# Performance work log

Hardware: AMD Instinct MI355X
Metric: run time of the kernel (lower is better)

The kernel has to match this reference:

```python
import jax, jax.numpy as jnp
import numpy as np

D = 8       # q_dim / embed dim
NF = 8      # num_feats
OUT = 8     # out_dim


def _get_emb(sin_inp):
    # interleaved sin/cos, matching positional_encodings.get_emb
    return jnp.stack([jnp.sin(sin_inp), jnp.cos(sin_inp)], axis=-1).reshape(sin_inp.shape[0], -1)


def pos_encoding_2d(X, Y, ch, dtype=jnp.float32):
    # PositionalEncoding2D over dims (X=window, Y=num_feats), channels=ch
    c = int(np.ceil(ch / 4) * 2)
    inv_freq = jnp.asarray((1.0 / (10000.0 ** (np.arange(0, c, 2) / np.float32(c)))).astype(np.float32))
    emb_x = _get_emb(jnp.arange(X, dtype=dtype)[:, None] * inv_freq[None, :])  # (X, c)
    emb_y = _get_emb(jnp.arange(Y, dtype=dtype)[:, None] * inv_freq[None, :])  # (Y, c)
    emb = jnp.zeros((X, Y, 2 * c), dtype)
    emb = emb.at[:, :, :c].set(emb_x[:, None, :])
    emb = emb.at[:, :, c:2 * c].set(emb_y[None, :, :])
    return emb[:, :, :ch]


def layer_norm(x, g, b, eps=1e-5):
    mu = jnp.mean(x, axis=-1, keepdims=True)
    var = jnp.mean((x - mu) ** 2, axis=-1, keepdims=True)
    return (x - mu) * jax.lax.rsqrt(var + eps) * g + b


def setup_inputs() -> dict:
    key = jax.random.key(0)
    ks = jax.random.split(key, 12)
    B, W = 128, 2048
    x = jax.random.normal(ks[0], (B, W, NF), dtype=jnp.float32)
    m = jax.random.randint(ks[1], (B, W, NF), 0, 2, dtype=jnp.int32)
    m = m.at[:, :, 0].set(0)  # guarantee at least one unmasked key per row
    s = 0.1
    return {
        "x": x,
        "m": m,
        "emb_w": jax.random.normal(ks[2], (D, 1), jnp.float32) * s,
        "emb_b": jax.random.normal(ks[3], (D,), jnp.float32) * s,
        "emb_ln_g": jnp.ones((D,), jnp.float32),
        "emb_ln_b": jnp.zeros((D,), jnp.float32),
        "ln_g": jnp.ones((D,), jnp.float32),
        "ln_b": jnp.zeros((D,), jnp.float32),
        "var_query": jax.random.normal(ks[4], (1, 1, D), jnp.float32) * s,
        "in_proj_w": jax.random.normal(ks[5], (3 * D, D), jnp.float32) * s,
        "in_proj_b": jax.random.normal(ks[6], (3 * D,), jnp.float32) * s,
        "out_proj_w": jax.random.normal(ks[7], (D, D), jnp.float32) * s,
        "out_proj_b": jax.random.normal(ks[8], (D,), jnp.float32) * s,
        "proj_w": jax.random.normal(ks[9], (OUT, D), jnp.float32) * s,
        "proj_b": jax.random.normal(ks[10], (OUT,), jnp.float32) * s,
    }


def reference(x, m, emb_w, emb_b, emb_ln_g, emb_ln_b, ln_g, ln_b, var_query,
              in_proj_w, in_proj_b, out_proj_w, out_proj_b, proj_w, proj_b):
    B, W, F = x.shape
    d = emb_w.shape[0]
    # LinearEmbed: Linear(1, d) on each scalar, then LayerNorm(d)
    h = x[..., None] * emb_w[:, 0] + emb_b              # (B, W, F, d)
    h = layer_norm(h, emb_ln_g, emb_ln_b)
    # 2D positional encoding over (window, feature) dims
    h = h + pos_encoding_2d(W, F, d)[None]
    # pre-attention LayerNorm
    h = layer_norm(h, ln_g, ln_b)
    # single-query multihead (1 head) cross attention, key_padding_mask = m
    Wq, Wk, Wv = in_proj_w[:d], in_proj_w[d:2 * d], in_proj_w[2 * d:]
    bq, bk, bv = in_proj_b[:d], in_proj_b[d:2 * d], in_proj_b[2 * d:]
    qv = Wq @ var_query.reshape(d) + bq                 # (d,) shared query
    k = jnp.einsum('bwfd,ed->bwfe', h, Wk) + bk         # (B, W, F, d)
    v = jnp.einsum('bwfd,ed->bwfe', h, Wv) + bv         # (B, W, F, d)
    logits = jnp.einsum('bwfe,e->bwf', k, qv) / jnp.sqrt(jnp.float32(d))
    logits = jnp.where(m.astype(bool), -jnp.inf, logits)
    attn_w = jax.nn.softmax(logits, axis=-1)            # (B, W, F)
    attn = jnp.einsum('bwf,bwfe->bwe', attn_w, v)       # (B, W, d)
    attn = attn @ out_proj_w.T + out_proj_b
    # final projection
    out = attn @ proj_w.T + proj_b                      # (B, W, OUT)
    return out
```

## Files before the change

kernel.cpp:

```cpp
#include <hip/hip_runtime.h>
#include <math.h>

#define THREADS 256
#define W_DIM 2048
#define INV_SQRT8 0.35355339059327373f

__global__ __launch_bounds__(THREADS) void misstsm_fused(
    const float* __restrict__ x, const int* __restrict__ m,
    const float* __restrict__ emb_w, const float* __restrict__ emb_b,
    const float* __restrict__ emb_ln_g, const float* __restrict__ emb_ln_b,
    const float* __restrict__ ln_g, const float* __restrict__ ln_b,
    const float* __restrict__ var_query,
    const float* __restrict__ in_proj_w, const float* __restrict__ in_proj_b,
    const float* __restrict__ out_proj_w, const float* __restrict__ out_proj_b,
    const float* __restrict__ proj_w, const float* __restrict__ proj_b,
    float* __restrict__ out, int npos)
{
    __shared__ float s_M[64];
    __shared__ float s_c2[8];
    __shared__ float s_a[8], s_bb[8], s_wlg[8], s_lg[8];
    __shared__ float s_Bf[32];
    __shared__ float s_sc[5];

    const int t = threadIdx.x;

    if (t < 64) {
        const int p = t >> 3, d = t & 7;
        float acc = 0.0f;
        #pragma unroll
        for (int e = 0; e < 8; ++e) {
            float po = 0.0f;
            #pragma unroll
            for (int o = 0; o < 8; ++o) po = fmaf(proj_w[p*8+o], out_proj_w[o*8+e], po);
            acc = fmaf(po, in_proj_w[(16+e)*8 + d], acc);
        }
        s_M[t] = acc;
    } else if (t < 72) {
        const int d = t - 64;
        float wk = 0.0f;
        #pragma unroll
        for (int e = 0; e < 8; ++e) {
            float qe = in_proj_b[e];
            #pragma unroll
            for (int dd = 0; dd < 8; ++dd) qe = fmaf(in_proj_w[e*8+dd], var_query[dd], qe);
            wk = fmaf(in_proj_w[(8+e)*8 + d], qe, wk);
        }
        s_wlg[d] = ln_g[d] * wk * INV_SQRT8;
        s_lg[d]  = ln_g[d];
    } else if (t < 80) {
        const int d = t - 72;
        float ewm = 0.0f, ebm = 0.0f;
        #pragma unroll
        for (int dd = 0; dd < 8; ++dd) { ewm += emb_w[dd]; ebm += emb_b[dd]; }
        ewm *= 0.125f; ebm *= 0.125f;
        s_a[d]  = (emb_w[d] - ewm) * emb_ln_g[d];
        s_bb[d] = (emb_b[d] - ebm) * emb_ln_g[d];
    } else if (t < 88) {
        const int p = t - 80;
        float c = proj_b[p];
        #pragma unroll
        for (int o = 0; o < 8; ++o) {
            float ob2 = out_proj_b[o];
            #pragma unroll
            for (int e = 0; e < 8; ++e) ob2 = fmaf(out_proj_w[o*8+e], in_proj_b[16+e], ob2);
            c = fmaf(proj_w[p*8+o], ob2, c);
        }
        #pragma unroll
        for (int e = 0; e < 8; ++e) {
            float po = 0.0f;
            #pragma unroll
            for (int o = 0; o < 8; ++o) po = fmaf(proj_w[p*8+o], out_proj_w[o*8+e], po);
            #pragma unroll
            for (int d = 0; d < 8; ++d)
                c = fmaf(po * in_proj_w[(16+e)*8 + d], ln_b[d], c);
        }
        s_c2[p] = c;
    } else if (t < 120) {
        const int k = t - 88, f = k >> 2, j = k & 3;
        const float ff = (float)f;
        float tr;
        if      (j == 0) tr = sinf(ff);
        else if (j == 1) tr = cosf(ff);
        else if (j == 2) tr = sinf(0.01f * ff);
        else             tr = cosf(0.01f * ff);
        s_Bf[k] = emb_ln_b[4 + j] + tr;
    } else if (t == 120) {
        float ewm = 0.0f, ebm = 0.0f;
        #pragma unroll
        for (int d = 0; d < 8; ++d) { ewm += emb_w[d]; ebm += emb_b[d]; }
        ewm *= 0.125f; ebm *= 0.125f;
        float A = 0.0f, Bc = 0.0f, Cc = 0.0f;
        #pragma unroll
        for (int d = 0; d < 8; ++d) {
            const float dw = emb_w[d] - ewm, db = emb_b[d] - ebm;
            A = fmaf(dw, dw, A); Bc = fmaf(dw, db, Bc); Cc = fmaf(db, db, Cc);
        }
        s_sc[0] = A * 0.125f;
        s_sc[1] = 2.0f * Bc * 0.125f;
        s_sc[2] = Cc * 0.125f + 1e-5f;
    } else if (t == 121) {
        float qv[8];
        float bkq = 0.0f;
        #pragma unroll
        for (int e = 0; e < 8; ++e) {
            float qe = in_proj_b[e];
            #pragma unroll
            for (int dd = 0; dd < 8; ++dd) qe = fmaf(in_proj_w[e*8+dd], var_query[dd], qe);
            qv[e] = qe;
            bkq = fmaf(in_proj_b[8+e], qe, bkq);
        }
        float swlg = 0.0f, ckd = 0.0f;
        #pragma unroll
        for (int d = 0; d < 8; ++d) {
            float wk = 0.0f;
            #pragma unroll
            for (int e = 0; e < 8; ++e) wk = fmaf(in_proj_w[(8+e)*8 + d], qv[e], wk);
            swlg = fmaf(ln_g[d], wk, swlg);
            ckd  = fmaf(ln_b[d], wk, ckd);
        }
        s_sc[3] = swlg * INV_SQRT8;
        s_sc[4] = (ckd + bkq) * INV_SQRT8;
    }
    __syncthreads();

    const int pos = blockIdx.x * THREADS + t;
    if (pos >= npos) return;
    const int w = pos & (W_DIM - 1);

    const float4* xv4 = reinterpret_cast<const float4*>(x);
    const int4*   mv4 = reinterpret_cast<const int4*>(m);
    const float4 xa = xv4[pos*2+0];
    const float4 xb = xv4[pos*2+1];
    const int4   ma = mv4[pos*2+0];
    const int4   mb = mv4[pos*2+1];

    const float xf[8] = {xa.x, xa.y, xa.z, xa.w, xb.x, xb.y, xb.z, xb.w};
    const int mk = (ma.x!=0?1:0) | (ma.y!=0?2:0) | (ma.z!=0?4:0) | (ma.w!=0?8:0)
                 | (mb.x!=0?16:0) | (mb.y!=0?32:0) | (mb.z!=0?64:0) | (mb.w!=0?128:0);

    const float fw = (float)w;
    float pB[4];
    pB[0] = emb_ln_b[0] + sinf(fw);
    pB[1] = emb_ln_b[1] + cosf(fw);
    pB[2] = emb_ln_b[2] + sinf(0.01f * fw);
    pB[3] = emb_ln_b[3] + cosf(0.01f * fw);

    const float A    = s_sc[0];
    const float twoB = s_sc[1];
    const float Cc   = s_sc[2];
    const float swlg = s_sc[3];
    const float cK   = s_sc[4];

    float av[8];
    #pragma unroll
    for (int d = 0; d < 8; ++d) av[d] = 0.0f;
    float S = 0.0f, smu = 0.0f;

    #pragma unroll
    for (int f = 0; f < 8; ++f) {
        const float xs = xf[f];
        const float r  = rsqrtf(fmaf(xs, fmaf(xs, A, twoB), Cc));
        const float tt = xs * r;
        float v[8];
        #pragma unroll
        for (int j = 0; j < 4; ++j)
            v[j] = fmaf(tt, s_a[j], fmaf(r, s_bb[j], pB[j]));
        #pragma unroll
        for (int j = 0; j < 4; ++j)
            v[4+j] = fmaf(tt, s_a[4+j], fmaf(r, s_bb[4+j], s_Bf[f*4 + j]));
        float sv = 0.0f, s2 = 0.0f, dt = 0.0f;
        #pragma unroll
        for (int d = 0; d < 8; ++d) {
            sv += v[d];
            s2  = fmaf(v[d], v[d], s2);
            dt  = fmaf(v[d], s_wlg[d], dt);
        }
        const float mu  = sv * 0.125f;
        const float var = fmaf(-mu, mu, fmaf(s2, 0.125f, 1e-5f));
        const float r2  = rsqrtf(var);
        const float l   = fmaf(r2, fmaf(-mu, swlg, dt), cK);
        const float e   = __expf(l);
        const float pp  = ((mk >> f) & 1) ? 0.0f : e;
        S += pp;
        const float cf = pp * r2;
        #pragma unroll
        for (int d = 0; d < 8; ++d) av[d] = fmaf(cf, v[d], av[d]);
        smu = fmaf(cf, mu, smu);
    }

    const float invS = 1.0f / S;
    float q[8];
    #pragma unroll
    for (int d = 0; d < 8; ++d) q[d] = s_lg[d] * invS * (av[d] - smu);

    float o[8];
    #pragma unroll
    for (int p = 0; p < 8; ++p) {
        float dp = s_c2[p];
        #pragma unroll
        for (int d = 0; d < 8; ++d) dp = fmaf(s_M[p*8+d], q[d], dp);
        o[p] = dp;
    }
    float4* ov4 = reinterpret_cast<float4*>(out);
    ov4[pos*2+0] = make_float4(o[0], o[1], o[2], o[3]);
    ov4[pos*2+1] = make_float4(o[4], o[5], o[6], o[7]);
}

extern "C" void kernel_launch(void* const* d_in, const int* in_sizes, int n_in,
                              void* d_out, int out_size, void* d_ws, size_t ws_size,
                              hipStream_t stream) {
    const float* x          = (const float*)d_in[0];
    const int*   m          = (const int*)d_in[1];
    const float* emb_w      = (const float*)d_in[2];
    const float* emb_b      = (const float*)d_in[3];
    const float* emb_ln_g   = (const float*)d_in[4];
    const float* emb_ln_b   = (const float*)d_in[5];
    const float* ln_g       = (const float*)d_in[6];
    const float* ln_b       = (const float*)d_in[7];
    const float* var_query  = (const float*)d_in[8];
    const float* in_proj_w  = (const float*)d_in[9];
    const float* in_proj_b  = (const float*)d_in[10];
    const float* out_proj_w = (const float*)d_in[11];
    const float* out_proj_b = (const float*)d_in[12];
    const float* proj_w     = (const float*)d_in[13];
    const float* proj_b     = (const float*)d_in[14];
    float* out = (float*)d_out;

    const int npos = in_sizes[0] / 8;
    const int grid = (npos + THREADS - 1) / THREADS;
    misstsm_fused<<<grid, THREADS, 0, stream>>>(
        x, m, emb_w, emb_b, emb_ln_g, emb_ln_b, ln_g, ln_b, var_query,
        in_proj_w, in_proj_b, out_proj_w, out_proj_b, proj_w, proj_b,
        out, npos);
}
```

Baseline: 16.00 us.

## Algebraically precompute LN statistics per feature and hoist global loads before setup

The per-feature second LayerNorm mean, variance and logit dot product are rewritten as closed-form polynomials in (tt, r), using per-block precomputed coefficients and per-feature tables in shared memory. This removes the 8-wide v vector and its reductions from the inner loop. The attention accumulator is kept as a few scalar sums and reassembled after the loop. The x/m global loads are also issued before the setup phase so they overlap with it, and sin/cos are merged into sincosf. The cost is more setup work per block, possible out-of-bounds loads for tail threads since the bounds check now comes after the loads, and variance computed by expansion, which risks cancellation.

```diff
diff --git a/kernel.cpp b/kernel.cpp
--- a/kernel.cpp
+++ b/kernel.cpp
@@ -19,113 +19,11 @@
     __shared__ float s_M[64];
     __shared__ float s_c2[8];
     __shared__ float s_a[8], s_bb[8], s_wlg[8], s_lg[8];
-    __shared__ float s_Bf[32];
-    __shared__ float s_sc[5];
+    __shared__ float s_F[8][12];
+    __shared__ float s_sc[12];
 
     const int t = threadIdx.x;
-
-    if (t < 64) {
-        const int p = t >> 3, d = t & 7;
-        float acc = 0.0f;
-        #pragma unroll
-        for (int e = 0; e < 8; ++e) {
-            float po = 0.0f;
-            #pragma unroll
-            for (int o = 0; o < 8; ++o) po = fmaf(proj_w[p*8+o], out_proj_w[o*8+e], po);
-            acc = fmaf(po, in_proj_w[(16+e)*8 + d], acc);
-        }
-        s_M[t] = acc;
-    } else if (t < 72) {
-        const int d = t - 64;
-        float wk = 0.0f;
-        #pragma unroll
-        for (int e = 0; e < 8; ++e) {
-            float qe = in_proj_b[e];
-            #pragma unroll
-            for (int dd = 0; dd < 8; ++dd) qe = fmaf(in_proj_w[e*8+dd], var_query[dd], qe);
-            wk = fmaf(in_proj_w[(8+e)*8 + d], qe, wk);
-        }
-        s_wlg[d] = ln_g[d] * wk * INV_SQRT8;
-        s_lg[d]  = ln_g[d];
-    } else if (t < 80) {
-        const int d = t - 72;
-        float ewm = 0.0f, ebm = 0.0f;
-        #pragma unroll
-        for (int dd = 0; dd < 8; ++dd) { ewm += emb_w[dd]; ebm += emb_b[dd]; }
-        ewm *= 0.125f; ebm *= 0.125f;
-        s_a[d]  = (emb_w[d] - ewm) * emb_ln_g[d];
-        s_bb[d] = (emb_b[d] - ebm) * emb_ln_g[d];
-    } else if (t < 88) {
-        const int p = t - 80;
-        float c = proj_b[p];
-        #pragma unroll
-        for (int o = 0; o < 8; ++o) {
-            float ob2 = out_proj_b[o];
-            #pragma unroll
-            for (int e = 0; e < 8; ++e) ob2 = fmaf(out_proj_w[o*8+e], in_proj_b[16+e], ob2);
-            c = fmaf(proj_w[p*8+o], ob2, c);
-        }
-        #pragma unroll
-        for (int e = 0; e < 8; ++e) {
-            float po = 0.0f;
-            #pragma unroll
-            for (int o = 0; o < 8; ++o) po = fmaf(proj_w[p*8+o], out_proj_w[o*8+e], po);
-            #pragma unroll
-            for (int d = 0; d < 8; ++d)
-                c = fmaf(po * in_proj_w[(16+e)*8 + d], ln_b[d], c);
-        }
-        s_c2[p] = c;
-    } else if (t < 120) {
-        const int k = t - 88, f = k >> 2, j = k & 3;
-        const float ff = (float)f;
-        float tr;
-        if      (j == 0) tr = sinf(ff);
-        else if (j == 1) tr = cosf(ff);
-        else if (j == 2) tr = sinf(0.01f * ff);
-        else             tr = cosf(0.01f * ff);
-        s_Bf[k] = emb_ln_b[4 + j] + tr;
-    } else if (t == 120) {
-        float ewm = 0.0f, ebm = 0.0f;
-        #pragma unroll
-        for (int d = 0; d < 8; ++d) { ewm += emb_w[d]; ebm += emb_b[d]; }
-        ewm *= 0.125f; ebm *= 0.125f;
-        float A = 0.0f, Bc = 0.0f, Cc = 0.0f;
-        #pragma unroll
-        for (int d = 0; d < 8; ++d) {
-            const float dw = emb_w[d] - ewm, db = emb_b[d] - ebm;
-            A = fmaf(dw, dw, A); Bc = fmaf(dw, db, Bc); Cc = fmaf(db, db, Cc);
-        }
-        s_sc[0] = A * 0.125f;
-        s_sc[1] = 2.0f * Bc * 0.125f;
-        s_sc[2] = Cc * 0.125f + 1e-5f;
-    } else if (t == 121) {
-        float qv[8];
-        float bkq = 0.0f;
-        #pragma unroll
-        for (int e = 0; e < 8; ++e) {
-            float qe = in_proj_b[e];
-            #pragma unroll
-            for (int dd = 0; dd < 8; ++dd) qe = fmaf(in_proj_w[e*8+dd], var_query[dd], qe);
-            qv[e] = qe;
-            bkq = fmaf(in_proj_b[8+e], qe, bkq);
-        }
-        float swlg = 0.0f, ckd = 0.0f;
-        #pragma unroll
-        for (int d = 0; d < 8; ++d) {
-            float wk = 0.0f;
-            #pragma unroll
-            for (int e = 0; e < 8; ++e) wk = fmaf(in_proj_w[(8+e)*8 + d], qv[e], wk);
-            swlg = fmaf(ln_g[d], wk, swlg);
-            ckd  = fmaf(ln_b[d], wk, ckd);
-        }
-        s_sc[3] = swlg * INV_SQRT8;
-        s_sc[4] = (ckd + bkq) * INV_SQRT8;
-    }
-    __syncthreads();
-
     const int pos = blockIdx.x * THREADS + t;
-    if (pos >= npos) return;
-    const int w = pos & (W_DIM - 1);
 
     const float4* xv4 = reinterpret_cast<const float4*>(x);
     const int4*   mv4 = reinterpret_cast<const int4*>(m);
@@ -134,64 +32,236 @@
     const int4   ma = mv4[pos*2+0];
     const int4   mb = mv4[pos*2+1];
 
+    if (t < 64) {
+        const int p = t >> 3, d = t & 7;
+        float acc = 0.0f;
+        #pragma unroll
+        for (int e = 0; e < 8; ++e) {
+            float po = 0.0f;
+            #pragma unroll
+            for (int o = 0; o < 8; ++o) po = fmaf(proj_w[p*8+o], out_proj_w[o*8+e], po);
+            acc = fmaf(po, in_proj_w[(16+e)*8 + d], acc);
+        }
+        s_M[t] = acc;
+    } else if (t < 72) {
+        const int d = t - 64;
+        float wk = 0.0f;
+        #pragma unroll
+        for (int e = 0; e < 8; ++e) {
+            float qe = in_proj_b[e];
+            #pragma unroll
+            for (int dd = 0; dd < 8; ++dd) qe = fmaf(in_proj_w[e*8+dd], var_query[dd], qe);
+            wk = fmaf(in_proj_w[(8+e)*8 + d], qe, wk);
+        }
+        s_wlg[d] = ln_g[d] * wk * INV_SQRT8;
+        s_lg[d]  = ln_g[d];
+    } else if (t < 80) {
+        const int d = t - 72;
+        float ewm = 0.0f, ebm = 0.0f;
+        #pragma unroll
+        for (int dd = 0; dd < 8; ++dd) { ewm += emb_w[dd]; ebm += emb_b[dd]; }
+        ewm *= 0.125f; ebm *= 0.125f;
+        s_a[d]  = (emb_w[d] - ewm) * emb_ln_g[d];
+        s_bb[d] = (emb_b[d] - ebm) * emb_ln_g[d];
+    } else if (t == 80) {
+        float ewm = 0.0f, ebm = 0.0f;
+        #pragma unroll
+        for (int d = 0; d < 8; ++d) { ewm += emb_w[d]; ebm += emb_b[d]; }
+        ewm *= 0.125f; ebm *= 0.125f;
+        float A = 0.0f, Bc = 0.0f, Cc = 0.0f;
+        #pragma unroll
+        for (int d = 0; d < 8; ++d) {
+            const float dw = emb_w[d] - ewm, db = emb_b[d] - ebm;
+            A = fmaf(dw, dw, A); Bc = fmaf(dw, db, Bc); Cc = fmaf(db, db, Cc);
+        }
+        s_sc[0] = A * 0.125f;
+        s_sc[1] = 2.0f * Bc * 0.125f;
+        s_sc[2] = Cc * 0.125f + 1e-5f;
+    } else if (t >= 128 && t < 136) {
+        const int p = t - 128;
+        float c = proj_b[p];
+        #pragma unroll
+        for (int o = 0; o < 8; ++o) {
+            float ob2 = out_proj_b[o];
+            #pragma unroll
+            for (int e = 0; e < 8; ++e) ob2 = fmaf(out_proj_w[o*8+e], in_proj_b[16+e], ob2);
+            c = fmaf(proj_w[p*8+o], ob2, c);
+        }
+        #pragma unroll
+        for (int e = 0; e < 8; ++e) {
+            float po = 0.0f;
+            #pragma unroll
+            for (int o = 0; o < 8; ++o) po = fmaf(proj_w[p*8+o], out_proj_w[o*8+e], po);
+            #pragma unroll
+            for (int d = 0; d < 8; ++d)
+                c = fmaf(po * in_proj_w[(16+e)*8 + d], ln_b[d], c);
+        }
+        s_c2[p] = c;
+    } else if (t == 136) {
+        float qv[8]; float bkq = 0.0f;
+        #pragma unroll
+        for (int e = 0; e < 8; ++e) {
+            float qe = in_proj_b[e];
+            #pragma unroll
+            for (int dd = 0; dd < 8; ++dd) qe = fmaf(in_proj_w[e*8+dd], var_query[dd], qe);
+            qv[e] = qe;
+            bkq = fmaf(in_proj_b[8+e], qe, bkq);
+        }
+        float ewm = 0.0f, ebm = 0.0f;
+        #pragma unroll
+        for (int d = 0; d < 8; ++d) { ewm += emb_w[d]; ebm += emb_b[d]; }
+        ewm *= 0.125f; ebm *= 0.125f;
+        float sa = 0, sb = 0, caa = 0, cbb = 0, cab = 0, ca = 0, cb = 0, sw = 0, ck = 0;
+        #pragma unroll
+        for (int d = 0; d < 8; ++d) {
+            const float ad = (emb_w[d] - ewm) * emb_ln_g[d];
+            const float bd = (emb_b[d] - ebm) * emb_ln_g[d];
+            float wk = 0.0f;
+            #pragma unroll
+            for (int e = 0; e < 8; ++e) wk = fmaf(in_proj_w[(8+e)*8 + d], qv[e], wk);
+            const float wl = ln_g[d] * wk * INV_SQRT8;
+            sa += ad; sb += bd;
+            caa = fmaf(ad, ad, caa); cbb = fmaf(bd, bd, cbb); cab = fmaf(ad, bd, cab);
+            ca  = fmaf(ad, wl, ca);  cb  = fmaf(bd, wl, cb);
+            sw += wl;
+            ck  = fmaf(ln_b[d], wk, ck);
+        }
+        s_sc[3]  = sw;
+        s_sc[4]  = (ck + bkq) * INV_SQRT8;
+        s_sc[5]  = sa * 0.125f;
+        s_sc[6]  = sb * 0.125f;
+        s_sc[7]  = caa * 0.125f;
+        s_sc[8]  = cbb * 0.125f;
+        s_sc[9]  = cab * 0.25f;
+        s_sc[10] = ca;
+        s_sc[11] = cb;
+    } else if (t >= 192 && t < 200) {
+        const int f = t - 192;
+        const float ff = (float)f;
+        float sy0, cy0, sy1, cy1;
+        sincosf(ff, &sy0, &cy0);
+        sincosf(0.01f * ff, &sy1, &cy1);
+        float Bf[4];
+        Bf[0] = emb_ln_b[4] + sy0; Bf[1] = emb_ln_b[5] + cy0;
+        Bf[2] = emb_ln_b[6] + sy1; Bf[3] = emb_ln_b[7] + cy1;
+        float ewm = 0.0f, ebm = 0.0f;
+        #pragma unroll
+        for (int d = 0; d < 8; ++d) { ewm += emb_w[d]; ebm += emb_b[d]; }
+        ewm *= 0.125f; ebm *= 0.125f;
+        float qv[8];
+        #pragma unroll
+        for (int e = 0; e < 8; ++e) {
+            float qe = in_proj_b[e];
+            #pragma unroll
+            for (int dd = 0; dd < 8; ++dd) qe = fmaf(in_proj_w[e*8+dd], var_query[dd], qe);
+            qv[e] = qe;
+        }
+        float bsum = 0, aB = 0, bB = 0, b2 = 0, bdot = 0;
+        #pragma unroll
+        for (int j = 0; j < 4; ++j) {
+            const int d = 4 + j;
+            const float ad = (emb_w[d] - ewm) * emb_ln_g[d];
+            const float bd = (emb_b[d] - ebm) * emb_ln_g[d];
+            float wk = 0.0f;
+            #pragma unroll
+            for (int e = 0; e < 8; ++e) wk = fmaf(in_proj_w[(8+e)*8 + d], qv[e], wk);
+            const float wl = ln_g[d] * wk * INV_SQRT8;
+            bsum += Bf[j];
+            aB  = fmaf(ad, Bf[j], aB);
+            bB  = fmaf(bd, Bf[j], bB);
+            b2  = fmaf(Bf[j], Bf[j], b2);
+            bdot = fmaf(wl, Bf[j], bdot);
+            s_F[f][j] = Bf[j];
+        }
+        s_F[f][4] = bsum * 0.125f;
+        s_F[f][5] = aB * 0.25f;
+        s_F[f][6] = bB * 0.25f;
+        s_F[f][7] = b2 * 0.125f;
+        s_F[f][8] = bdot;
+    }
+    __syncthreads();
+
+    if (pos >= npos) return;
+    const int w = pos & (W_DIM - 1);
+
     const float xf[8] = {xa.x, xa.y, xa.z, xa.w, xb.x, xb.y, xb.z, xb.w};
     const int mk = (ma.x!=0?1:0) | (ma.y!=0?2:0) | (ma.z!=0?4:0) | (ma.w!=0?8:0)
                  | (mb.x!=0?16:0) | (mb.y!=0?32:0) | (mb.z!=0?64:0) | (mb.w!=0?128:0);
 
+    const float A    = s_sc[0], twoB = s_sc[1], Cc  = s_sc[2];
+    const float swlg = s_sc[3], cK   = s_sc[4];
+    const float sa8  = s_sc[5], sb8  = s_sc[6];
+    const float caa8 = s_sc[7], cbb8 = s_sc[8], cab8 = s_sc[9];
+    const float ca   = s_sc[10], cb  = s_sc[11];
+
     const float fw = (float)w;
+    float s1, c1, sl, clo;
+    sincosf(fw, &s1, &c1);
+    sincosf(0.01f * fw, &sl, &clo);
     float pB[4];
-    pB[0] = emb_ln_b[0] + sinf(fw);
-    pB[1] = emb_ln_b[1] + cosf(fw);
-    pB[2] = emb_ln_b[2] + sinf(0.01f * fw);
-    pB[3] = emb_ln_b[3] + cosf(0.01f * fw);
-
-    const float A    = s_sc[0];
-    const float twoB = s_sc[1];
-    const float Cc   = s_sc[2];
-    const float swlg = s_sc[3];
-    const float cK   = s_sc[4];
-
-    float av[8];
-    #pragma unroll
-    for (int d = 0; d < 8; ++d) av[d] = 0.0f;
-    float S = 0.0f, smu = 0.0f;
+    pB[0] = emb_ln_b[0] + s1;  pB[1] = emb_ln_b[1] + c1;
+    pB[2] = emb_ln_b[2] + sl;  pB[3] = emb_ln_b[3] + clo;
+
+    float pBsum = 0, apB = 0, bpB = 0, pB2 = 0, pBdot = 0;
+    #pragma unroll
+    for (int j = 0; j < 4; ++j) {
+        pBsum += pB[j];
+        apB  = fmaf(s_a[j],  pB[j], apB);
+        bpB  = fmaf(s_bb[j], pB[j], bpB);
+        pB2  = fmaf(pB[j],  pB[j], pB2);
+        pBdot = fmaf(s_wlg[j], pB[j], pBdot);
+    }
+    const float pBsum8  = pBsum * 0.125f;
+    const float twoapB8 = apB * 0.25f;
+    const float twobpB8 = bpB * 0.25f;
+    const float pB28eps = fmaf(pB2, 0.125f, 1e-5f);
+
+    float S = 0, SC = 0, ctt = 0, crr = 0, smu = 0;
+    float avB[4] = {0, 0, 0, 0};
 
     #pragma unroll
     for (int f = 0; f < 8; ++f) {
+        const float F0 = s_F[f][0], F1 = s_F[f][1], F2 = s_F[f][2], F3 = s_F[f][3];
+        const float F4 = s_F[f][4], F5 = s_F[f][5], F6 = s_F[f][6], F7 = s_F[f][7];
+        const float F8 = s_F[f][8];
         const float xs = xf[f];
         const float r  = rsqrtf(fmaf(xs, fmaf(xs, A, twoB), Cc));
         const float tt = xs * r;
-        float v[8];
-        #pragma unroll
-        for (int j = 0; j < 4; ++j)
-            v[j] = fmaf(tt, s_a[j], fmaf(r, s_bb[j], pB[j]));
-        #pragma unroll
-        for (int j = 0; j < 4; ++j)
-            v[4+j] = fmaf(tt, s_a[4+j], fmaf(r, s_bb[4+j], s_Bf[f*4 + j]));
-        float sv = 0.0f, s2 = 0.0f, dt = 0.0f;
-        #pragma unroll
-        for (int d = 0; d < 8; ++d) {
-            sv += v[d];
-            s2  = fmaf(v[d], v[d], s2);
-            dt  = fmaf(v[d], s_wlg[d], dt);
-        }
-        const float mu  = sv * 0.125f;
-        const float var = fmaf(-mu, mu, fmaf(s2, 0.125f, 1e-5f));
+        const float mu = fmaf(tt, sa8, fmaf(r, sb8, pBsum8 + F4));
+        const float e1 = twoapB8 + F5;
+        const float e2 = twobpB8 + F6;
+        const float e3 = pB28eps + F7;
+        const float s2v = fmaf(tt, fmaf(tt, caa8, fmaf(r, cab8, e1)),
+                               fmaf(r, fmaf(r, cbb8, e2), e3));
+        const float var = fmaf(-mu, mu, s2v);
         const float r2  = rsqrtf(var);
+        const float dt  = fmaf(tt, ca, fmaf(r, cb, pBdot + F8));
         const float l   = fmaf(r2, fmaf(-mu, swlg, dt), cK);
         const float e   = __expf(l);
         const float pp  = ((mk >> f) & 1) ? 0.0f : e;
-        S += pp;
-        const float cf = pp * r2;
-        #pragma unroll
-        for (int d = 0; d < 8; ++d) av[d] = fmaf(cf, v[d], av[d]);
+        const float cf  = pp * r2;
+        S += pp; SC += cf;
+        ctt = fmaf(cf, tt, ctt);
+        crr = fmaf(cf, r,  crr);
         smu = fmaf(cf, mu, smu);
+        avB[0] = fmaf(cf, F0, avB[0]);
+        avB[1] = fmaf(cf, F1, avB[1]);
+        avB[2] = fmaf(cf, F2, avB[2]);
+        avB[3] = fmaf(cf, F3, avB[3]);
     }
 
     const float invS = 1.0f / S;
     float q[8];
     #pragma unroll
-    for (int d = 0; d < 8; ++d) q[d] = s_lg[d] * invS * (av[d] - smu);
+    for (int j = 0; j < 4; ++j) {
+        const float av = fmaf(ctt, s_a[j], fmaf(crr, s_bb[j], SC * pB[j]));
+        q[j] = s_lg[j] * invS * (av - smu);
+    }
+    #pragma unroll
+    for (int j = 0; j < 4; ++j) {
+        const float av = fmaf(ctt, s_a[4+j], fmaf(crr, s_bb[4+j], avB[j]));
+        q[4+j] = s_lg[4+j] * invS * (av - smu);
+    }
 
     float o[8];
     #pragma unroll
```

Measured after the change: 13.93 us. 12.9% less time.
